# Kernel optimization log

Hardware: AMD Instinct MI355X
Metric: run time of the kernel (lower is better)

## Reference

```python
import jax, jax.numpy as jnp
import numpy as np

N_NODES = 100000
N_EDGES = 1600000
F_IN, HID = 256, 256
HID_OUT = HID // 2  # last SAGE layer output


def _glorot(key, shape):
    fan_in, fan_out = shape[1], shape[0]
    lim = (6.0 / (fan_in + fan_out)) ** 0.5
    return jax.random.uniform(key, shape, jnp.float32, -lim, lim)


def setup_inputs() -> dict:
    key = jax.random.key(0)
    ks = jax.random.split(key, 12)
    x = jax.random.normal(ks[0], (N_NODES, F_IN), jnp.float32)
    edge_index = jax.random.randint(ks[1], (2, N_EDGES), 0, N_NODES, jnp.int64)
    # SAGEConv params: lin_l (on aggregated neighbors, has bias), lin_r (on root)
    dims = [(F_IN, HID), (HID, HID), (HID, HID_OUT)]
    inp = {"x": x, "edge_index": edge_index}
    for i, (din, dout) in enumerate(dims):
        inp[f"Wl{i}"] = _glorot(ks[2 + 3 * i], (dout, din))
        inp[f"Wr{i}"] = _glorot(ks[3 + 3 * i], (dout, din))
        inp[f"b{i}"] = jnp.zeros((dout,), jnp.float32)
    inp["Wc"] = _glorot(ks[11], (1, HID_OUT))
    inp["bc"] = jnp.zeros((1,), jnp.float32)
    return inp


def _sage_conv(x, src, dst, Wl, Wr, b):
    # mean aggregation of source features at destination nodes
    msg_sum = jax.ops.segment_sum(x[src], dst, num_segments=N_NODES)  # [N, d]
    deg = jax.ops.segment_sum(jnp.ones((src.shape[0], 1), x.dtype), dst,
                              num_segments=N_NODES)  # [N, 1]
    agg = msg_sum / jnp.maximum(deg, 1.0)
    return agg @ Wl.T + x @ Wr.T + b


def reference(x, edge_index, Wl0, Wr0, b0, Wl1, Wr1, b1, Wl2, Wr2, b2, Wc, bc):
    src, dst = edge_index[0], edge_index[1]
    layers = [(Wl0, Wr0, b0), (Wl1, Wr1, b1), (Wl2, Wr2, b2)]
    h = x
    for i, (Wl, Wr, b) in enumerate(layers):
        h = _sage_conv(h, src, dst, Wl, Wr, b)
        if i < len(layers) - 1:
            h = jax.nn.relu(h)  # dropout is identity in eval mode
    return jax.nn.sigmoid(h @ Wc.T + bc)  # [N, 1]
```

## Files before the change

### kernel.cpp

```cpp
#include <hip/hip_runtime.h>
#include <math.h>

#define N_NODES 100000
#define N_PAD   100352
#define N_EDGES 1600000
#define DIN 256

#define NB 782
#define NC 256
#define CHUNK 6250
#define MT_N (NB * NC)
#define MT_PAD 200448

typedef unsigned short u16;
typedef unsigned char u8;
typedef unsigned int u32;
typedef __attribute__((ext_vector_type(8))) short bf16x8;
typedef __attribute__((ext_vector_type(8))) unsigned short us8;
typedef __attribute__((ext_vector_type(4))) float f32x4;
typedef __attribute__((ext_vector_type(2))) float f32x2;

__device__ __forceinline__ float b2f(u16 u) {
    union { unsigned int i; float f; } c; c.i = ((unsigned int)u) << 16; return c.f;
}
__device__ __forceinline__ u16 f2b(float f) {
    union { float f; unsigned int i; } c; c.f = f;
    unsigned int x = c.i;
    return (u16)((x + 0x7fffu + ((x >> 16) & 1u)) >> 16);
}
__device__ __forceinline__ u8 f32_to_fp8(float v) {
    return (u8)(__builtin_amdgcn_cvt_pk_fp8_f32(v, 0.0f, 0, false) & 0xff);
}
__device__ __forceinline__ void accum16(float* a, uint4 v) {
    unsigned int w[4] = { v.x, v.y, v.z, v.w };
    #pragma unroll
    for (int q = 0; q < 4; ++q) {
        f32x2 lo = __builtin_amdgcn_cvt_pk_f32_fp8(w[q], false);
        f32x2 hi = __builtin_amdgcn_cvt_pk_f32_fp8(w[q], true);
        a[q * 4 + 0] += lo[0]; a[q * 4 + 1] += lo[1];
        a[q * 4 + 2] += hi[0]; a[q * 4 + 3] += hi[1];
    }
}
__device__ __forceinline__ void accum8(float* a, uint2 v) {
    unsigned int w[2] = { v.x, v.y };
    #pragma unroll
    for (int q = 0; q < 2; ++q) {
        f32x2 lo = __builtin_amdgcn_cvt_pk_f32_fp8(w[q], false);
        f32x2 hi = __builtin_amdgcn_cvt_pk_f32_fp8(w[q], true);
        a[q * 4 + 0] += lo[0]; a[q * 4 + 1] += lo[1];
        a[q * 4 + 2] += hi[0]; a[q * 4 + 3] += hi[1];
    }
}

__device__ __forceinline__ void gload_lds16(const u16* g, u16* lds_base) {
    __builtin_amdgcn_global_load_lds(
        (const __attribute__((address_space(1))) void*)g,
        (__attribute__((address_space(3))) void*)lds_base, 16, 0, 0);
}

__device__ __forceinline__ u32 xcd_chunk(u32 orig, u32 nwg) {
    u32 q = nwg >> 3, r = nwg & 7;
    u32 xcd = orig & 7, idx = orig >> 3;
    u32 base = (xcd < r) ? xcd * (q + 1) : r * (q + 1) + (xcd - r) * q;
    return base + idx;
}

__global__ void cvt_kernel(const float* __restrict__ in, u16* __restrict__ outb,
                           u8* __restrict__ out8, int n4) {
    int i = blockIdx.x * blockDim.x + threadIdx.x;
    if (i < n4) {
        float4 v = ((const float4*)in)[i];
        ushort4 o;
        o.x = f2b(v.x); o.y = f2b(v.y); o.z = f2b(v.z); o.w = f2b(v.w);
        ((ushort4*)outb)[i] = o;
        u32 r = __builtin_amdgcn_cvt_pk_fp8_f32(v.x, v.y, 0, false);
        r = __builtin_amdgcn_cvt_pk_fp8_f32(v.z, v.w, r, true);
        ((u32*)out8)[i] = r;
    }
}

__global__ void cvtw_kernel(const float* __restrict__ Wl0, const float* __restrict__ Wr0,
                            const float* __restrict__ Wl1, const float* __restrict__ Wr1,
                            const float* __restrict__ Wl2, const float* __restrict__ Wr2,
                            u16* __restrict__ wl0, u16* __restrict__ wr0,
                            u16* __restrict__ wl1, u16* __restrict__ wr1,
                            u16* __restrict__ wl2, u16* __restrict__ wr2) {
    int b = blockIdx.x;
    const float* s; u16* d; int i;
    if (b < 64)       { s = Wl0; d = wl0; i = b * 256 + threadIdx.x; }
    else if (b < 128) { s = Wr0; d = wr0; i = (b - 64) * 256 + threadIdx.x; }
    else if (b < 192) { s = Wl1; d = wl1; i = (b - 128) * 256 + threadIdx.x; }
    else if (b < 256) { s = Wr1; d = wr1; i = (b - 192) * 256 + threadIdx.x; }
    else if (b < 288) { s = Wl2; d = wl2; i = (b - 256) * 256 + threadIdx.x; }
    else              { s = Wr2; d = wr2; i = (b - 288) * 256 + threadIdx.x; }
    float4 v = ((const float4*)s)[i];
    ushort4 o;
    o.x = f2b(v.x); o.y = f2b(v.y); o.z = f2b(v.z); o.w = f2b(v.w);
    ((ushort4*)d)[i] = o;
}

__launch_bounds__(256)
__global__ void p1_hist(const int* __restrict__ dst, int* __restrict__ MT) {
    __shared__ int bins[NB];
    const int c = blockIdx.x, tid = threadIdx.x;
    for (int b = tid; b < NB; b += 256) bins[b] = 0;
    __syncthreads();
    const int e0 = c * CHUNK;
    for (int e = e0 + tid; e < e0 + CHUNK; e += 256)
        atomicAdd(&bins[dst[e] >> 7], 1);
    __syncthreads();
    for (int b = tid; b < NB; b += 256) MT[b * NC + c] = bins[b];
}

__global__ void scan1_kernel(const int* __restrict__ in, int* __restrict__ excl,
                             int* __restrict__ blocksums, int n) {
    __shared__ int s[256];
    int tid = threadIdx.x;
    int i = blockIdx.x * 256 + tid;
    int v = (i < n) ? in[i] : 0;
    s[tid] = v;
    __syncthreads();
    for (int off = 1; off < 256; off <<= 1) {
        int t = (tid >= off) ? s[tid - off] : 0;
        __syncthreads();
        s[tid] += t;
        __syncthreads();
    }
    if (i < n) excl[i] = s[tid] - v;
    if (tid == 255) blocksums[blockIdx.x] = s[255];
}

__global__ void scan_carry_kernel(int* __restrict__ bsums, int nb) {
    __shared__ int s[256];
    int tid = threadIdx.x;
    int carry = 0;
    for (int base = 0; base < nb; base += 256) {
        int i = base + tid;
        int v = (i < nb) ? bsums[i] : 0;
        s[tid] = v;
        __syncthreads();
        for (int off = 1; off < 256; off <<= 1) {
            int t = (tid >= off) ? s[tid - off] : 0;
            __syncthreads();
            s[tid] += t;
            __syncthreads();
        }
        int incl = s[tid];
        int tot = s[255];
        if (i < nb) bsums[i] = incl - v + carry;
        carry += tot;
        __syncthreads();
    }
}

__global__ void scan3_kernel(int* __restrict__ excl, const int* __restrict__ blocksums, int n) {
    int i = blockIdx.x * 256 + threadIdx.x;
    if (i < n) excl[i] += blocksums[blockIdx.x];
}

__launch_bounds__(256)
__global__ void p2_partition(const int* __restrict__ src, const int* __restrict__ dst,
                             const int* __restrict__ scanMT, u32* __restrict__ csr_tmp) {
    __shared__ int cur[NB];
    const int c = blockIdx.x, tid = threadIdx.x;
    for (int b = tid; b < NB; b += 256) cur[b] = scanMT[b * NC + c];
    __syncthreads();
    const int e0 = c * CHUNK;
    for (int e = e0 + tid; e < e0 + CHUNK; e += 256) {
        int d = dst[e];
        int pos = atomicAdd(&cur[d >> 7], 1);
        csr_tmp[pos] = ((u32)(d & 127) << 25) | (u32)src[e];
    }
}

__launch_bounds__(256)
__global__ void p3_csr(const int* __restrict__ scanMT, const u32* __restrict__ csr_tmp,
                       int* __restrict__ csr, int* __restrict__ rowptr,
                       int* __restrict__ rowend, float* __restrict__ rinv) {
    __shared__ int cnt[128];
    __shared__ int excl[128];
    __shared__ int cur[128];
    const int b = blockIdx.x, tid = threadIdx.x;
    const int beg = scanMT[b * NC];
    const int end = (b == NB - 1) ? N_EDGES : scanMT[(b + 1) * NC];
    if (tid < 128) cnt[tid] = 0;
    __syncthreads();
    for (int e = beg + tid; e < end; e += 256)
        atomicAdd(&cnt[csr_tmp[e] >> 25], 1);
    __syncthreads();
    if (tid == 0) {
        int run = 0;
        for (int i = 0; i < 128; ++i) { excl[i] = run; run += cnt[i]; }
    }
    __syncthreads();
    if (tid < 128) cur[tid] = beg + excl[tid];
    __syncthreads();
    for (int e = beg + tid; e < end; e += 256) {
        u32 v = csr_tmp[e];
        int pos = atomicAdd(&cur[v >> 25], 1);
        csr[pos] = (int)(v & 0x1FFFFFFu);
    }
    if (tid < 128) {
        int node = b * 128 + tid;
        if (node < N_NODES) {
            int rp = beg + excl[tid];
            rowptr[node] = rp;
            rowend[node] = rp + cnt[tid];
            rinv[node]   = 1.0f / (float)max(cnt[tid], 1);
        }
    }
}

__launch_bounds__(256)
__global__ void agg_kernel(const int* __restrict__ rowptr, const int* __restrict__ rowend,
                           const int* __restrict__ csr_src, const float* __restrict__ rinv,
                           const u8* __restrict__ h8, u16* __restrict__ agg) {
    int node = blockIdx.x * 16 + (threadIdx.x >> 4);
    int lane = threadIdx.x & 15;
    if (node >= N_NODES) return;
    int beg = rowptr[node];
    int end = rowend[node];
    const u8* hl = h8 + lane * 16;
    float a[16] = {};
    int p = beg;
    for (; p + 3 < end; p += 4) {
        int s0 = csr_src[p], s1 = csr_src[p + 1], s2 = csr_src[p + 2], s3 = csr_src[p + 3];
        uint4 v0 = *(const uint4*)(hl + (size_t)s0 * 256);
        uint4 v1 = *(const uint4*)(hl + (size_t)s1 * 256);
        uint4 v2 = *(const uint4*)(hl + (size_t)s2 * 256);
        uint4 v3 = *(const uint4*)(hl + (size_t)s3 * 256);
        accum16(a, v0); accum16(a, v1); accum16(a, v2); accum16(a, v3);
    }
    for (; p < end; ++p) {
        uint4 v0 = *(const uint4*)(hl + (size_t)csr_src[p] * 256);
        accum16(a, v0);
    }
    float r = rinv[node];
    us8 o0, o1;
    #pragma unroll
    for (int j = 0; j < 8; ++j) { o0[j] = f2b(a[j] * r); o1[j] = f2b(a[8 + j] * r); }
    u16* d = agg + (size_t)node * DIN + lane * 16;
    *(us8*)d = o0;
    *(us8*)(d + 8) = o1;
}

template <int MODE>
__launch_bounds__(256)
__global__ void sage_gemm(const u16* __restrict__ A0, const u16* __restrict__ A1,
                          const u16* __restrict__ B0w, const u16* __restrict__ B1w,
                          const float* __restrict__ bias, void* __restrict__ out0,
                          void* __restrict__ out1, u8* __restrict__ out8,
                          int dout, int do_relu) {
    __shared__ u16 sA[2][128 * 32];
    __shared__ u16 sB[2][128 * 32];

    const u32 u    = xcd_chunk(blockIdx.x, gridDim.x);
    const int csel = u & 1;
    const int row0 = (int)(u >> 1) * 128;
    const int col0 = (MODE == 0) ? csel * 128 : 0;
    const int t    = threadIdx.x;
    const int w    = t >> 6, lane = t & 63;
    const int wr   = w >> 1, wc = w & 1;
    const int lr   = lane & 15, lg = lane >> 4;
    const int srow = lane >> 2;
    const int sblk = (lane & 3) ^ ((lane >> 3) & 3);
    const u16* Bsel = csel ? B1w : B0w;

    f32x4 acc[4][4] = {};
    const int NT = (MODE == 0) ? 16 : 8;

    auto stage = [&](int buf, int tk) {
        const int kt = tk * 32;
        const u16* Asrc = (MODE == 0 && kt >= 256) ? A1 : A0;
        const u16* Bsrc = (MODE == 0) ? ((kt >= 256) ? B1w : B0w) : Bsel;
        const int  kb   = (MODE == 0 && kt >= 256) ? kt - 256 : kt;
        #pragma unroll
        for (int i = 0; i < 2; ++i) {
            int row = w * 32 + i * 16 + srow;
            gload_lds16(Asrc + (size_t)(row0 + row) * DIN + kb + sblk * 8,
                        &sA[buf][w * 1024 + i * 512]);
            gload_lds16(Bsrc + (size_t)(col0 + row) * DIN + kb + sblk * 8,
                        &sB[buf][w * 1024 + i * 512]);
        }
    };

    stage(0, 0);
    stage(1, 1);
    for (int tk = 0; tk < NT; ++tk) {
        const int cur = tk & 1;
        if (tk + 1 < NT) asm volatile("s_waitcnt vmcnt(4)" ::: "memory");
        else             asm volatile("s_waitcnt vmcnt(0)" ::: "memory");
        __builtin_amdgcn_sched_barrier(0);
        __builtin_amdgcn_s_barrier();

        bf16x8 af[4], bfr[4];
        #pragma unroll
        for (int m = 0; m < 4; ++m) {
            int row = wr * 64 + m * 16 + lr;
            af[m] = *(const bf16x8*)&sA[cur][row * 32 + 8 * (lg ^ ((lr >> 1) & 3))];
        }
        #pragma unroll
        for (int n = 0; n < 4; ++n) {
            int row = wc * 64 + n * 16 + lr;
            bfr[n] = *(const bf16x8*)&sB[cur][row * 32 + 8 * (lg ^ ((lr >> 1) & 3))];
        }
        #pragma unroll
        for (int m = 0; m < 4; ++m)
            #pragma unroll
            for (int n = 0; n < 4; ++n)
                acc[m][n] = __builtin_amdgcn_mfma_f32_16x16x32_bf16(af[m], bfr[n], acc[m][n], 0, 0, 0);

        asm volatile("s_waitcnt lgkmcnt(0)" ::: "memory");
        __builtin_amdgcn_sched_barrier(0);
        __builtin_amdgcn_s_barrier();
        if (tk + 2 < NT) stage(cur, tk + 2);
    }

    const bool f32out = (MODE == 1) && (csel == 1);
    #pragma unroll
    for (int m = 0; m < 4; ++m) {
        int row = row0 + wr * 64 + m * 16 + lg * 4;
        #pragma unroll
        for (int n = 0; n < 4; ++n) {
            int col = col0 + wc * 64 + n * 16 + lr;
            #pragma unroll
            for (int r = 0; r < 4; ++r) {
                float v = acc[m][n][r];
                if (MODE == 0) {
                    v += bias[col];
                    if (do_relu) v = fmaxf(v, 0.0f);
                    ((u16*)out0)[(size_t)(row + r) * dout + col] = f2b(v);
                    if (out8) out8[(size_t)(row + r) * dout + col] = f32_to_fp8(v);
                } else if (f32out) {
                    v += bias[col];
                    ((float*)out1)[(size_t)(row + r) * dout + col] = v;
                } else {
                    out8[(size_t)(row + r) * dout + col] = f32_to_fp8(v);
                }
            }
        }
    }
}

__launch_bounds__(256)
__global__ void aggcls_kernel(const int* __restrict__ rowptr, const int* __restrict__ rowend,
                              const int* __restrict__ csr_src, const float* __restrict__ rinv,
                              const u8* __restrict__ z28, const float* __restrict__ y2,
                              const float* __restrict__ Wc, const float* __restrict__ bc,
                              float* __restrict__ out) {
    __shared__ float sW[128];
    int t = threadIdx.x;
    if (t < 128) sW[t] = Wc[t];
    __syncthreads();
    int node = blockIdx.x * 16 + (t >> 4);
    int lane = t & 15;
    if (node >= N_NODES) return;
    int beg = rowptr[node];
    int end = rowend[node];
    const u8* zl = z28 + lane * 8;
    float a[8] = {};
    int p = beg;
    for (; p + 3 < end; p += 4) {
        int s0 = csr_src[p], s1 = csr_src[p + 1], s2 = csr_src[p + 2], s3 = csr_src[p + 3];
        uint2 v0 = *(const uint2*)(zl + (size_t)s0 * 128);
        uint2 v1 = *(const uint2*)(zl + (size_t)s1 * 128);
        uint2 v2 = *(const uint2*)(zl + (size_t)s2 * 128);
        uint2 v3 = *(const uint2*)(zl + (size_t)s3 * 128);
        accum8(a, v0); accum8(a, v1); accum8(a, v2); accum8(a, v3);
    }
    for (; p < end; ++p) {
        uint2 v0 = *(const uint2*)(zl + (size_t)csr_src[p] * 128);
        accum8(a, v0);
    }
    float r = rinv[node];
    float4 ylo = *(const float4*)(y2 + (size_t)node * 128 + lane * 8);
    float4 yhi = *(const float4*)(y2 + (size_t)node * 128 + lane * 8 + 4);
    float yv[8] = { ylo.x, ylo.y, ylo.z, ylo.w, yhi.x, yhi.y, yhi.z, yhi.w };
    float s = 0.f;
    #pragma unroll
    for (int j = 0; j < 8; ++j)
        s += (a[j] * r + yv[j]) * sW[lane * 8 + j];
    #pragma unroll
    for (int off = 8; off; off >>= 1) s += __shfl_xor(s, off, 16);
    if (lane == 0) {
        float z = s + bc[0];
        out[node] = 1.0f / (1.0f + expf(-z));
    }
}

extern "C" void kernel_launch(void* const* d_in, const int* in_sizes, int n_in,
                              void* d_out, int out_size, void* d_ws, size_t ws_size,
                              hipStream_t stream) {
    const float* x   = (const float*)d_in[0];
    const int*   ei  = (const int*)d_in[1];
    const float* Wl0 = (const float*)d_in[2];
    const float* Wr0 = (const float*)d_in[3];
    const float* b0  = (const float*)d_in[4];
    const float* Wl1 = (const float*)d_in[5];
    const float* Wr1 = (const float*)d_in[6];
    const float* b1  = (const float*)d_in[7];
    const float* Wl2 = (const float*)d_in[8];
    const float* Wr2 = (const float*)d_in[9];
    const float* b2  = (const float*)d_in[10];
    const float* Wc  = (const float*)d_in[11];
    const float* bc  = (const float*)d_in[12];
    float* out = (float*)d_out;

    const int* src = ei;
    const int* dst = ei + N_EDGES;

    int*   MT     = (int*)d_ws;
    int*   MTs    = MT + MT_PAD;
    int*   bsums  = MTs + MT_PAD;
    u32*   csrtmp = (u32*)(bsums + 1024);
    int*   csr    = (int*)(csrtmp + N_EDGES);
    int*   rowptr = csr + N_EDGES;
    int*   rowend = rowptr + N_PAD;
    float* rinv   = (float*)(rowend + N_PAD);
    u16*   xb     = (u16*)(rinv + N_PAD);
    u16*   wb     = xb + (size_t)N_PAD * 256;
    u16*   bufA   = wb + 327680;
    u16*   bufB   = bufA + (size_t)N_PAD * 256;
    u16*   bufC   = bufB + (size_t)N_PAD * 256;
    u8*    x8     = (u8*)(bufC + (size_t)N_PAD * 256);
    u8*    h18    = x8 + (size_t)N_PAD * 256;
    u8*    z28    = h18 + (size_t)N_PAD * 256;

    u16* wl0 = wb;
    u16* wr0 = wl0 + 65536;
    u16* wl1 = wr0 + 65536;
    u16* wr1 = wl1 + 65536;
    u16* wl2 = wr1 + 65536;
    u16* wr2 = wl2 + 32768;

    cvt_kernel<<<(N_NODES * 64 + 255) / 256, 256, 0, stream>>>(x, xb, x8, N_NODES * 64);
    cvtw_kernel<<<320, 256, 0, stream>>>(Wl0, Wr0, Wl1, Wr1, Wl2, Wr2,
                                         wl0, wr0, wl1, wr1, wl2, wr2);

    const int scan_blocks = (MT_N + 255) / 256;
    p1_hist<<<NC, 256, 0, stream>>>(dst, MT);
    scan1_kernel<<<scan_blocks, 256, 0, stream>>>(MT, MTs, bsums, MT_N);
    scan_carry_kernel<<<1, 256, 0, stream>>>(bsums, scan_blocks);
    scan3_kernel<<<scan_blocks, 256, 0, stream>>>(MTs, bsums, MT_N);
    p2_partition<<<NC, 256, 0, stream>>>(src, dst, MTs, csrtmp);
    p3_csr<<<NB, 256, 0, stream>>>(MTs, csrtmp, csr, rowptr, rowend, rinv);

    const int Mblocks = (N_NODES + 127) / 128;
    const int gemm_blocks = Mblocks * 2;
    const int agg_blocks = (N_NODES + 15) / 16;

    agg_kernel<<<agg_blocks, 256, 0, stream>>>(rowptr, rowend, csr, rinv, x8, bufA);
    sage_gemm<0><<<gemm_blocks, 256, 0, stream>>>(bufA, xb, wl0, wr0, b0, bufB, nullptr, h18, 256, 1);

    agg_kernel<<<agg_blocks, 256, 0, stream>>>(rowptr, rowend, csr, rinv, h18, bufA);
    sage_gemm<0><<<gemm_blocks, 256, 0, stream>>>(bufA, bufB, wl1, wr1, b1, bufC, nullptr, nullptr, 256, 1);

    sage_gemm<1><<<gemm_blocks, 256, 0, stream>>>(bufC, nullptr, wl2, wr2, b2, nullptr, bufB, z28, 128, 0);
    aggcls_kernel<<<agg_blocks, 256, 0, stream>>>(rowptr, rowend, csr, rinv,
                                                  z28, (const float*)bufB, Wc, bc, out);
}
```

Measured before the change: 421.9 us.

## Widen GEMM tile to full 256 output columns and merge conversion kernels

The SAGE GEMM now has each block compute a 128x256 tile covering every output column, instead of two 128x128 column halves. Each A row tile is therefore loaded once rather than twice, and the XCD chunk remapping is removed. The x and weight conversion kernels are also merged into one launch. The cost is a doubled accumulator count per thread (more registers and lower occupancy), more LDS for the B tile, and half as many blocks (782) to spread across the CUs.

```diff
diff --git a/kernel.cpp b/kernel.cpp
--- a/kernel.cpp
+++ b/kernel.cpp
@@ -58,34 +58,29 @@
         (__attribute__((address_space(3))) void*)lds_base, 16, 0, 0);
 }
 
-__device__ __forceinline__ u32 xcd_chunk(u32 orig, u32 nwg) {
-    u32 q = nwg >> 3, r = nwg & 7;
-    u32 xcd = orig & 7, idx = orig >> 3;
-    u32 base = (xcd < r) ? xcd * (q + 1) : r * (q + 1) + (xcd - r) * q;
-    return base + idx;
-}
-
-__global__ void cvt_kernel(const float* __restrict__ in, u16* __restrict__ outb,
-                           u8* __restrict__ out8, int n4) {
-    int i = blockIdx.x * blockDim.x + threadIdx.x;
-    if (i < n4) {
-        float4 v = ((const float4*)in)[i];
-        ushort4 o;
-        o.x = f2b(v.x); o.y = f2b(v.y); o.z = f2b(v.z); o.w = f2b(v.w);
-        ((ushort4*)outb)[i] = o;
-        u32 r = __builtin_amdgcn_cvt_pk_fp8_f32(v.x, v.y, 0, false);
-        r = __builtin_amdgcn_cvt_pk_fp8_f32(v.z, v.w, r, true);
-        ((u32*)out8)[i] = r;
-    }
-}
-
-__global__ void cvtw_kernel(const float* __restrict__ Wl0, const float* __restrict__ Wr0,
-                            const float* __restrict__ Wl1, const float* __restrict__ Wr1,
-                            const float* __restrict__ Wl2, const float* __restrict__ Wr2,
-                            u16* __restrict__ wl0, u16* __restrict__ wr0,
-                            u16* __restrict__ wl1, u16* __restrict__ wr1,
-                            u16* __restrict__ wl2, u16* __restrict__ wr2) {
+__global__ void cvt_kernel(const float* __restrict__ x, u16* __restrict__ xb,
+                           u8* __restrict__ x8, int xblocks,
+                           const float* __restrict__ Wl0, const float* __restrict__ Wr0,
+                           const float* __restrict__ Wl1, const float* __restrict__ Wr1,
+                           const float* __restrict__ Wl2, const float* __restrict__ Wr2,
+                           u16* __restrict__ wl0, u16* __restrict__ wr0,
+                           u16* __restrict__ wl1, u16* __restrict__ wr1,
+                           u16* __restrict__ wl2, u16* __restrict__ wr2) {
     int b = blockIdx.x;
+    if (b < xblocks) {
+        int i = b * 256 + threadIdx.x;
+        if (i < N_NODES * 64) {
+            float4 v = ((const float4*)x)[i];
+            ushort4 o;
+            o.x = f2b(v.x); o.y = f2b(v.y); o.z = f2b(v.z); o.w = f2b(v.w);
+            ((ushort4*)xb)[i] = o;
+            u32 r = __builtin_amdgcn_cvt_pk_fp8_f32(v.x, v.y, 0, false);
+            r = __builtin_amdgcn_cvt_pk_fp8_f32(v.z, v.w, r, true);
+            ((u32*)x8)[i] = r;
+        }
+        return;
+    }
+    b -= xblocks;
     const float* s; u16* d; int i;
     if (b < 64)       { s = Wl0; d = wl0; i = b * 256 + threadIdx.x; }
     else if (b < 128) { s = Wr0; d = wr0; i = (b - 64) * 256 + threadIdx.x; }
@@ -250,37 +245,39 @@
                           const u16* __restrict__ B0w, const u16* __restrict__ B1w,
                           const float* __restrict__ bias, void* __restrict__ out0,
                           void* __restrict__ out1, u8* __restrict__ out8,
-                          int dout, int do_relu) {
+                          int do_relu) {
     __shared__ u16 sA[2][128 * 32];
-    __shared__ u16 sB[2][128 * 32];
-
-    const u32 u    = xcd_chunk(blockIdx.x, gridDim.x);
-    const int csel = u & 1;
-    const int row0 = (int)(u >> 1) * 128;
-    const int col0 = (MODE == 0) ? csel * 128 : 0;
+    __shared__ u16 sB[2][256 * 32];
+
+    const int row0 = blockIdx.x * 128;
     const int t    = threadIdx.x;
     const int w    = t >> 6, lane = t & 63;
     const int wr   = w >> 1, wc = w & 1;
     const int lr   = lane & 15, lg = lane >> 4;
     const int srow = lane >> 2;
     const int sblk = (lane & 3) ^ ((lane >> 3) & 3);
-    const u16* Bsel = csel ? B1w : B0w;
-
-    f32x4 acc[4][4] = {};
+
+    f32x4 acc[4][8] = {};
     const int NT = (MODE == 0) ? 16 : 8;
 
     auto stage = [&](int buf, int tk) {
         const int kt = tk * 32;
         const u16* Asrc = (MODE == 0 && kt >= 256) ? A1 : A0;
-        const u16* Bsrc = (MODE == 0) ? ((kt >= 256) ? B1w : B0w) : Bsel;
         const int  kb   = (MODE == 0 && kt >= 256) ? kt - 256 : kt;
         #pragma unroll
         for (int i = 0; i < 2; ++i) {
             int row = w * 32 + i * 16 + srow;
             gload_lds16(Asrc + (size_t)(row0 + row) * DIN + kb + sblk * 8,
                         &sA[buf][w * 1024 + i * 512]);
-            gload_lds16(Bsrc + (size_t)(col0 + row) * DIN + kb + sblk * 8,
-                        &sB[buf][w * 1024 + i * 512]);
+        }
+        #pragma unroll
+        for (int i = 0; i < 4; ++i) {
+            int row = w * 64 + i * 16 + srow;
+            const u16* bp;
+            if (MODE == 0) bp = ((kt >= 256) ? B1w : B0w) + (size_t)row * DIN + kb;
+            else           bp = (row < 128 ? B0w + (size_t)row * DIN
+                                           : B1w + (size_t)(row - 128) * DIN) + kb;
+            gload_lds16(bp + sblk * 8, &sB[buf][w * 2048 + i * 512]);
         }
     };
 
@@ -288,26 +285,26 @@
     stage(1, 1);
     for (int tk = 0; tk < NT; ++tk) {
         const int cur = tk & 1;
-        if (tk + 1 < NT) asm volatile("s_waitcnt vmcnt(4)" ::: "memory");
+        if (tk + 1 < NT) asm volatile("s_waitcnt vmcnt(6)" ::: "memory");
         else             asm volatile("s_waitcnt vmcnt(0)" ::: "memory");
         __builtin_amdgcn_sched_barrier(0);
         __builtin_amdgcn_s_barrier();
 
-        bf16x8 af[4], bfr[4];
+        bf16x8 af[4], bfr[8];
         #pragma unroll
         for (int m = 0; m < 4; ++m) {
             int row = wr * 64 + m * 16 + lr;
             af[m] = *(const bf16x8*)&sA[cur][row * 32 + 8 * (lg ^ ((lr >> 1) & 3))];
         }
         #pragma unroll
-        for (int n = 0; n < 4; ++n) {
-            int row = wc * 64 + n * 16 + lr;
+        for (int n = 0; n < 8; ++n) {
+            int row = wc * 128 + n * 16 + lr;
             bfr[n] = *(const bf16x8*)&sB[cur][row * 32 + 8 * (lg ^ ((lr >> 1) & 3))];
         }
         #pragma unroll
         for (int m = 0; m < 4; ++m)
             #pragma unroll
-            for (int n = 0; n < 4; ++n)
+            for (int n = 0; n < 8; ++n)
                 acc[m][n] = __builtin_amdgcn_mfma_f32_16x16x32_bf16(af[m], bfr[n], acc[m][n], 0, 0, 0);
 
         asm volatile("s_waitcnt lgkmcnt(0)" ::: "memory");
@@ -316,26 +313,24 @@
         if (tk + 2 < NT) stage(cur, tk + 2);
     }
 
-    const bool f32out = (MODE == 1) && (csel == 1);
     #pragma unroll
     for (int m = 0; m < 4; ++m) {
         int row = row0 + wr * 64 + m * 16 + lg * 4;
         #pragma unroll
-        for (int n = 0; n < 4; ++n) {
-            int col = col0 + wc * 64 + n * 16 + lr;
+        for (int n = 0; n < 8; ++n) {
+            int col = wc * 128 + n * 16 + lr;
             #pragma unroll
             for (int r = 0; r < 4; ++r) {
                 float v = acc[m][n][r];
                 if (MODE == 0) {
                     v += bias[col];
                     if (do_relu) v = fmaxf(v, 0.0f);
-                    ((u16*)out0)[(size_t)(row + r) * dout + col] = f2b(v);
-                    if (out8) out8[(size_t)(row + r) * dout + col] = f32_to_fp8(v);
-                } else if (f32out) {
-                    v += bias[col];
-                    ((float*)out1)[(size_t)(row + r) * dout + col] = v;
+                    ((u16*)out0)[(size_t)(row + r) * 256 + col] = f2b(v);
+                    if (out8) out8[(size_t)(row + r) * 256 + col] = f32_to_fp8(v);
+                } else if (col < 128) {
+                    out8[(size_t)(row + r) * 128 + col] = f32_to_fp8(v);
                 } else {
-                    out8[(size_t)(row + r) * dout + col] = f32_to_fp8(v);
+                    ((float*)out1)[(size_t)(row + r) * 128 + (col - 128)] = v + bias[col - 128];
                 }
             }
         }
@@ -433,9 +428,10 @@
     u16* wl2 = wr1 + 65536;
     u16* wr2 = wl2 + 32768;
 
-    cvt_kernel<<<(N_NODES * 64 + 255) / 256, 256, 0, stream>>>(x, xb, x8, N_NODES * 64);
-    cvtw_kernel<<<320, 256, 0, stream>>>(Wl0, Wr0, Wl1, Wr1, Wl2, Wr2,
-                                         wl0, wr0, wl1, wr1, wl2, wr2);
+    const int xblocks = (N_NODES * 64 + 255) / 256;
+    cvt_kernel<<<xblocks + 320, 256, 0, stream>>>(x, xb, x8, xblocks,
+                                                  Wl0, Wr0, Wl1, Wr1, Wl2, Wr2,
+                                                  wl0, wr0, wl1, wr1, wl2, wr2);
 
     const int scan_blocks = (MT_N + 255) / 256;
     p1_hist<<<NC, 256, 0, stream>>>(dst, MT);
@@ -446,16 +442,15 @@
     p3_csr<<<NB, 256, 0, stream>>>(MTs, csrtmp, csr, rowptr, rowend, rinv);
 
     const int Mblocks = (N_NODES + 127) / 128;
-    const int gemm_blocks = Mblocks * 2;
     const int agg_blocks = (N_NODES + 15) / 16;
 
     agg_kernel<<<agg_blocks, 256, 0, stream>>>(rowptr, rowend, csr, rinv, x8, bufA);
-    sage_gemm<0><<<gemm_blocks, 256, 0, stream>>>(bufA, xb, wl0, wr0, b0, bufB, nullptr, h18, 256, 1);
+    sage_gemm<0><<<Mblocks, 256, 0, stream>>>(bufA, xb, wl0, wr0, b0, bufB, nullptr, h18, 1);
 
     agg_kernel<<<agg_blocks, 256, 0, stream>>>(rowptr, rowend, csr, rinv, h18, bufA);
-    sage_gemm<0><<<gemm_blocks, 256, 0, stream>>>(bufA, bufB, wl1, wr1, b1, bufC, nullptr, nullptr, 256, 1);
-
-    sage_gemm<1><<<gemm_blocks, 256, 0, stream>>>(bufC, nullptr, wl2, wr2, b2, nullptr, bufB, z28, 128, 0);
+    sage_gemm<0><<<Mblocks, 256, 0, stream>>>(bufA, bufB, wl1, wr1, b1, bufC, nullptr, nullptr, 1);
+
+    sage_gemm<1><<<Mblocks, 256, 0, stream>>>(bufC, nullptr, wl2, wr2, b2, nullptr, bufB, z28, 0);
     aggcls_kernel<<<agg_blocks, 256, 0, stream>>>(rowptr, rowend, csr, rinv,
                                                   z28, (const float*)bufB, Wc, bc, out);
 }
```

Result: slower. 497.2 us (+17.9%).
